# Optimization experiments

Measured on AMD Instinct MI355X. Metric: run time of the kernel, lower is better.

Reference implementation:

```python
import jax, jax.numpy as jnp
import numpy as np

N = 20000   # nodes
E = 160000  # edges
IN = 16     # in_channels
H = 32      # hidden_channels
MID = 32    # edge-MLP hidden width


def setup_inputs() -> dict:
    key = jax.random.key(0)
    ks = jax.random.split(key, 18)
    s = 0.1  # param scale
    return {
        "x": jax.random.normal(ks[0], (N, IN), jnp.float32),
        "edge_index": jax.random.randint(ks[1], (2, E), 0, N, dtype=jnp.int64),
        "edge_weight": jax.random.uniform(ks[2], (E,), jnp.float32),
        # edge_net1: Linear(1,32) -> SiLU -> Linear(32, IN*H)
        "en1_w1": jax.random.normal(ks[3], (1, MID), jnp.float32) * s,
        "en1_b1": jax.random.normal(ks[4], (MID,), jnp.float32) * s,
        "en1_w2": jax.random.normal(ks[5], (MID, IN * H), jnp.float32) * s,
        "en1_b2": jax.random.normal(ks[6], (IN * H,), jnp.float32) * s,
        "root1": jax.random.normal(ks[7], (IN, H), jnp.float32) * s,
        "bias1": jax.random.normal(ks[8], (H,), jnp.float32) * s,
        # edge_net2: Linear(1,32) -> SiLU -> Linear(32, H*H)
        "en2_w1": jax.random.normal(ks[9], (1, MID), jnp.float32) * s,
        "en2_b1": jax.random.normal(ks[10], (MID,), jnp.float32) * s,
        "en2_w2": jax.random.normal(ks[11], (MID, H * H), jnp.float32) * s,
        "en2_b2": jax.random.normal(ks[12], (H * H,), jnp.float32) * s,
        "root2": jax.random.normal(ks[13], (H, H), jnp.float32) * s,
        "bias2": jax.random.normal(ks[14], (H,), jnp.float32) * s,
        "dec_w": jax.random.normal(ks[15], (H, 1), jnp.float32) * s,
        "dec_b": jax.random.normal(ks[16], (1,), jnp.float32) * s,
    }


def _nnconv(x, src, dst, inv_cnt, e, w1, b1, w2, b2, root, bias, cin, cout):
    # edge MLP -> per-edge [cin, cout] weight matrix
    h = jax.nn.silu(e @ w1 + b1)            # [E, MID]
    w = (h @ w2 + b2).reshape(-1, cin, cout)  # [E, cin, cout]
    msg = jnp.einsum('ei,eio->eo', x[src], w)  # per-edge matmul [E, cout]
    agg = jax.ops.segment_sum(msg, dst, num_segments=N) * inv_cnt  # scatter-mean
    return agg + x @ root + bias


def reference(x, edge_index, edge_weight,
              en1_w1, en1_b1, en1_w2, en1_b2, root1, bias1,
              en2_w1, en2_b1, en2_w2, en2_b2, root2, bias2,
              dec_w, dec_b):
    src, dst = edge_index[0], edge_index[1]
    e = edge_weight[:, None]  # [E, 1]
    cnt = jax.ops.segment_sum(jnp.ones((E,), x.dtype), dst, num_segments=N)
    inv_cnt = (1.0 / jnp.maximum(cnt, 1.0))[:, None]  # [N, 1]
    h = _nnconv(x, src, dst, inv_cnt, e, en1_w1, en1_b1, en1_w2, en1_b2, root1, bias1, IN, H)
    h = jax.nn.silu(h)
    h = _nnconv(h, src, dst, inv_cnt, e, en2_w1, en2_b1, en2_w2, en2_b2, root2, bias2, H, H)
    h = jax.nn.silu(h)
    out = h @ dec_w + dec_b  # [N, 1]
    return out[:, 0]
```

## Files before the change

### kernel.cpp

```cpp
#include <hip/hip_runtime.h>
#include <hip/hip_bf16.h>

#define NN 20000
#define EE 160000
#define HH 32
#define MIDD 32

typedef _Float16 f16x4 __attribute__((ext_vector_type(4)));
typedef _Float16 f16x8 __attribute__((ext_vector_type(8)));
typedef float f32x4 __attribute__((ext_vector_type(4)));

__device__ __forceinline__ float silu_f(float v) {
    return __fdividef(v, 1.0f + __expf(-v));
}

__device__ __forceinline__ void gload_lds_b32(const void* gsrc, void* ldst) {
    __builtin_amdgcn_global_load_lds(
        (const __attribute__((address_space(1))) void*)gsrc,
        (__attribute__((address_space(3))) void*)ldst, 4, 0, 0);
}


__global__ void count_kernel(const int* __restrict__ ei, int* __restrict__ cnt) {
    int e = blockIdx.x * 256 + threadIdx.x;
    if (e < EE) atomicAdd(&cnt[ei[EE + e]], 1);
}

__global__ __launch_bounds__(1024) void scan_kernel(
    const int* __restrict__ cnt, int* __restrict__ off,
    int* __restrict__ cur, float* __restrict__ invc) {
    const int t = threadIdx.x;
    const int base = t * 20;
    __shared__ int wtot[16];

    int c[20];
    if (base + 20 <= NN) {
        const int4* p = (const int4*)(cnt + base);
        #pragma unroll
        for (int q = 0; q < 5; ++q) *(int4*)&c[4 * q] = p[q];
    } else {
        #pragma unroll
        for (int r = 0; r < 20; ++r) {
            int idx = base + r;
            c[r] = (idx < NN) ? cnt[idx] : 0;
        }
    }

    int loc[20];
    int s = 0;
    #pragma unroll
    for (int r = 0; r < 20; ++r) { loc[r] = s; s += c[r]; }

    const int lane = t & 63, wv = t >> 6;
    int incl = s;
    #pragma unroll
    for (int d2 = 1; d2 < 64; d2 <<= 1) {
        int u = __shfl_up(incl, d2);
        if (lane >= d2) incl += u;
    }
    if (lane == 63) wtot[wv] = incl;
    __syncthreads();
    int wbase = 0;
    for (int p2 = 0; p2 < wv; ++p2) wbase += wtot[p2];

    const int excl = wbase + incl - s;

    int o[20];
    #pragma unroll
    for (int r = 0; r < 20; ++r) o[r] = excl + loc[r];
    float iv[20];
    #pragma unroll
    for (int r = 0; r < 20; ++r) iv[r] = 1.0f / fmaxf((float)c[r], 1.0f);

    if (base + 20 <= NN) {
        #pragma unroll
        for (int q = 0; q < 5; ++q) {
            ((int4*)(off + base))[q]    = *(const int4*)&o[4 * q];
            ((int4*)(cur + base))[q]    = *(const int4*)&o[4 * q];
            ((float4*)(invc + base))[q] = *(const float4*)&iv[4 * q];
        }
    } else {
        #pragma unroll
        for (int r = 0; r < 20; ++r) {
            int idx = base + r;
            if (idx < NN) { off[idx] = o[r]; cur[idx] = o[r]; invc[idx] = iv[r]; }
        }
    }
    if (t == 0) off[NN] = EE;
}

__global__ void scatter_kernel(const int* __restrict__ ei, const float* __restrict__ ewt,
                               int* __restrict__ cur,
                               int* __restrict__ ssrc, float* __restrict__ sew) {
    int e = blockIdx.x * 256 + threadIdx.x;
    if (e < EE) {
        int d = ei[EE + e];
        int pos = atomicAdd(&cur[d], 1);
        ssrc[pos] = ei[e];
        sew[pos] = ewt[e];
    }
}

__global__ void build_wt(const float* __restrict__ w2a, const float* __restrict__ b2a,
                         const float* __restrict__ ra,
                         const float* __restrict__ w2b, const float* __restrict__ b2b,
                         const float* __restrict__ rb,
                         const float* __restrict__ x,
                         _Float16* __restrict__ Wt1, _Float16* __restrict__ Wt2,
                         _Float16* __restrict__ x16) {
    int idx = blockIdx.x * 256 + threadIdx.x;
    if (idx < 17408) {
        int o = idx / 544, k = idx % 544;
        float v;
        if (k < 512) {
            int m = k & 31, i = k >> 5;
            v = w2a[m * 512 + i * 32 + o];
        } else if (k < 528) {
            v = b2a[(k - 512) * 32 + o];
        } else {
            v = ra[(k - 528) * 32 + o];
        }
        Wt1[o * 544 + k] = (_Float16)v;
    } else if (idx < 52224) {
        int j = idx - 17408;
        int o = j / 1088, k = j % 1088;
        float v;
        if (k < 1024) {
            int m = k & 31, i = k >> 5;
            v = w2b[m * 1024 + i * 32 + o];
        } else if (k < 1056) {
            v = b2b[(k - 1024) * 32 + o];
        } else {
            v = rb[(k - 1056) * 32 + o];
        }
        Wt2[o * 1088 + k] = (_Float16)v;
    } else if (idx < 52224 + NN * 16) {
        int j = idx - 52224;
        x16[j] = (_Float16)x[j];
    }
}


template <int CIN, bool DECODE>
__global__ __launch_bounds__(512, 6) void fused_layer(
    const _Float16* __restrict__ xin16, const int* __restrict__ ssrc,
    const float* __restrict__ sew, const int* __restrict__ off,
    const float* __restrict__ invc, const float* __restrict__ w1,
    const float* __restrict__ b1, const _Float16* __restrict__ Wt,
    const float* __restrict__ bias, void* __restrict__ outp,
    const float* __restrict__ dw, const float* __restrict__ db) {
    constexpr int K = 34 * CIN;
    constexpr int LDK = K + 4;
    constexpr int JS = (32 * CIN) / 64;
    constexpr int NH = JS / 8;
    constexpr int steps = K / 32;
    constexpr int CAP = 192;
    constexpr int RPG = 128 / CIN;
    constexpr int LPR = CIN / 2;

    extern __shared__ char smem[];
    _Float16* Fl = (_Float16*)smem;
    float* pool = (float*)(smem + (size_t)16 * LDK * 2);
    int*   Is = (int*)pool;
    float* Es = pool + CAP;
    _Float16* Xs = (_Float16*)(pool + 2 * CAP);
    float* red = pool;

    const int t = threadIdx.x;
    const int n0 = blockIdx.x * 16;
    const int lane = t & 63, w = t >> 6;

    const int E0 = off[n0];
    const int E1 = off[n0 + 16];
    const int L = E1 - E0;
    const int Lc = (L < CAP) ? L : CAP;

    if (w == 0) {
        for (int c = 0; c < Lc; c += 64) {
            int idx = c + lane; idx = (idx < L - 1) ? idx : (L - 1);
            gload_lds_b32(ssrc + E0 + idx, Is + c);
        }
    } else if (w == 1) {
        for (int c = 0; c < Lc; c += 64) {
            int idx = c + lane; idx = (idx < L - 1) ? idx : (L - 1);
            gload_lds_b32(sew + E0 + idx, Es + c);
        }
    }
    __syncthreads();

    {
        const int G = (Lc + RPG - 1) / RPG;
        const int er = lane / LPR;
        const int ecp = lane % LPR;
        for (int p = w; p < G; p += 8) {
            int el = p * RPG + er; el = (el < Lc - 1) ? el : (Lc - 1);
            int sn = Is[el];
            gload_lds_b32(xin16 + (size_t)sn * CIN + 2 * ecp,
                          Xs + (size_t)p * RPG * CIN);
        }
    }
    __syncthreads();

    {
        const int m = lane & 31;
        const int ihalf = (lane >> 5) * JS;
        const int i0 = lane & (CIN - 1);
        const float w1v = w1[m];
        const float b1v = b1[m];

        for (int c = 0; c < 2; ++c) {
            const int nsub = w * 2 + c;
            const int d = n0 + nsub;
            float Sacc[JS];
            #pragma unroll
            for (int j = 0; j < JS; ++j) Sacc[j] = 0.f;
            float S0 = 0.f;

            const int e0l = off[d] - E0, e1l = off[d + 1] - E0;
            const int eL = (e1l < Lc) ? e1l : Lc;
            const float iv = invc[d];

            #pragma unroll 2
            for (int el = e0l; el < eL; ++el) {
                const float ew = Es[el];
                const float hv = silu_f(fmaf(ew, w1v, b1v));
                const int rb = el * CIN;
                f16x8 xh[NH];
                #pragma unroll
                for (int q = 0; q < NH; ++q)
                    xh[q] = *(const f16x8*)&Xs[rb + ihalf + 8 * q];
                #pragma unroll
                for (int q = 0; q < NH; ++q)
                    #pragma unroll
                    for (int j = 0; j < 8; ++j)
                        Sacc[8 * q + j] = fmaf((float)xh[q][j], hv, Sacc[8 * q + j]);
                S0 += (float)Xs[rb + i0];
            }
            for (int el = eL; el < e1l; ++el) {
                const int sn2 = ssrc[E0 + el];
                const float ew2 = sew[E0 + el];
                const float hv2 = silu_f(fmaf(ew2, w1v, b1v));
                const _Float16* xrow = xin16 + (size_t)sn2 * CIN;
                #pragma unroll
                for (int q = 0; q < NH; ++q) {
                    f16x8 xq = *(const f16x8*)(xrow + ihalf + 8 * q);
                    #pragma unroll
                    for (int j = 0; j < 8; ++j)
                        Sacc[8 * q + j] = fmaf((float)xq[j], hv2, Sacc[8 * q + j]);
                }
                S0 += (float)xrow[i0];
            }

            _Float16* Fr = Fl + (size_t)nsub * LDK;
            #pragma unroll
            for (int j = 0; j < JS; ++j)
                Fr[(ihalf + j) * 32 + m] = (_Float16)(Sacc[j] * iv);
            if (lane < CIN)
                Fr[32 * CIN + lane] = (_Float16)(S0 * iv);
            else if (lane < 2 * CIN)
                Fr[32 * CIN + lane] = xin16[(size_t)d * CIN + (lane - CIN)];
        }
    }
    __syncthreads();

    const int o16 = lane & 15, g = lane >> 4;

    const _Float16* Arow = Fl + (size_t)o16 * LDK + g * 4;
    const _Float16* B0 = Wt + (size_t)o16 * K + g * 4;
    const _Float16* B1 = Wt + (size_t)(o16 + 16) * K + g * 4;

    f32x4 acc0 = {0.f, 0.f, 0.f, 0.f};
    f32x4 acc1 = {0.f, 0.f, 0.f, 0.f};

    const int sb = (steps * w) >> 3;
    const int se = (steps * (w + 1)) >> 3;
    #pragma unroll 2
    for (int s = sb; s < se; ++s) {
        const int k0 = s * 32;
        f16x4 alo = *(const f16x4*)(Arow + k0);
        f16x4 ahi = *(const f16x4*)(Arow + k0 + 16);
        f16x4 b0l = *(const f16x4*)(B0 + k0);
        f16x4 b0h = *(const f16x4*)(B0 + k0 + 16);
        f16x4 b1l = *(const f16x4*)(B1 + k0);
        f16x4 b1h = *(const f16x4*)(B1 + k0 + 16);
        f16x8 a, bb0, bb1;
        #pragma unroll
        for (int j = 0; j < 4; ++j) {
            a[j] = alo[j];  a[j + 4] = ahi[j];
            bb0[j] = b0l[j]; bb0[j + 4] = b0h[j];
            bb1[j] = b1l[j]; bb1[j + 4] = b1h[j];
        }
        acc0 = __builtin_amdgcn_mfma_f32_16x16x32_f16(a, bb0, acc0, 0, 0, 0);
        acc1 = __builtin_amdgcn_mfma_f32_16x16x32_f16(a, bb1, acc1, 0, 0, 0);
    }

    if (w > 0) {
        float* rw = red + (w - 1) * 512;
        #pragma unroll
        for (int r = 0; r < 4; ++r) {
            rw[(g * 4 + r) * 32 + o16]      = acc0[r];
            rw[(g * 4 + r) * 32 + 16 + o16] = acc1[r];
        }
    }
    __syncthreads();
    if (w == 0) {
        #pragma unroll
        for (int r = 0; r < 4; ++r) {
            const int ro = (g * 4 + r) * 32 + o16;
            #pragma unroll
            for (int p = 0; p < 7; ++p) {
                acc0[r] += red[p * 512 + ro];
                acc1[r] += red[p * 512 + ro + 16];
            }
        }
        const float bb0 = bias[o16], bb1 = bias[o16 + 16];
        const int nrow = n0 + g * 4;
        if (!DECODE) {
            _Float16* op = (_Float16*)outp;
            #pragma unroll
            for (int r = 0; r < 4; ++r) {
                op[(size_t)(nrow + r) * 32 + o16]      = (_Float16)silu_f(acc0[r] + bb0);
                op[(size_t)(nrow + r) * 32 + 16 + o16] = (_Float16)silu_f(acc1[r] + bb1);
            }
        } else {
            float* op = (float*)outp;
            const float w0 = dw[o16], w1v = dw[o16 + 16];
            const float dbv = db[0];
            #pragma unroll
            for (int r = 0; r < 4; ++r) {
                float p = silu_f(acc0[r] + bb0) * w0 + silu_f(acc1[r] + bb1) * w1v;
                p += __shfl_xor(p, 1);
                p += __shfl_xor(p, 2);
                p += __shfl_xor(p, 4);
                p += __shfl_xor(p, 8);
                if (o16 == 0) op[nrow + r] = p + dbv;
            }
        }
    }
}


extern "C" void kernel_launch(void* const* d_in, const int* in_sizes, int n_in,
                              void* d_out, int out_size, void* d_ws, size_t ws_size,
                              hipStream_t stream) {
    const float* x      = (const float*)d_in[0];
    const int*   ei     = (const int*)d_in[1];
    const float* ew     = (const float*)d_in[2];
    const float* en1_w1 = (const float*)d_in[3];
    const float* en1_b1 = (const float*)d_in[4];
    const float* en1_w2 = (const float*)d_in[5];
    const float* en1_b2 = (const float*)d_in[6];
    const float* root1  = (const float*)d_in[7];
    const float* bias1  = (const float*)d_in[8];
    const float* en2_w1 = (const float*)d_in[9];
    const float* en2_b1 = (const float*)d_in[10];
    const float* en2_w2 = (const float*)d_in[11];
    const float* en2_b2 = (const float*)d_in[12];
    const float* root2  = (const float*)d_in[13];
    const float* bias2  = (const float*)d_in[14];
    const float* dec_w  = (const float*)d_in[15];
    const float* dec_b  = (const float*)d_in[16];
    float* out = (float*)d_out;
    (void)in_sizes; (void)n_in; (void)out_size; (void)ws_size;

    char* wp = (char*)d_ws;
    auto alloc = [&](size_t bytes) {
        char* p = wp;
        wp += (bytes + 255) & ~(size_t)255;
        return p;
    };
    int*      cnt  = (int*)alloc((size_t)NN * 4);
    int*      off  = (int*)alloc((size_t)(NN + 1) * 4);
    int*      cur  = (int*)alloc((size_t)NN * 4);
    float*    invc = (float*)alloc((size_t)NN * 4);
    int*      ssrc = (int*)alloc((size_t)EE * 4);
    float*    sew  = (float*)alloc((size_t)EE * 4);
    _Float16* h1h  = (_Float16*)alloc((size_t)NN * 32 * 2);
    _Float16* x16  = (_Float16*)alloc((size_t)NN * 16 * 2);
    _Float16* Wt1  = (_Float16*)alloc((size_t)17408 * 2);
    _Float16* Wt2  = (_Float16*)alloc((size_t)34816 * 2);

    hipMemsetAsync(cnt, 0, (size_t)NN * 4, stream);

    count_kernel<<<(EE + 255) / 256, 256, 0, stream>>>(ei, cnt);
    scan_kernel<<<1, 1024, 0, stream>>>(cnt, off, cur, invc);
    scatter_kernel<<<(EE + 255) / 256, 256, 0, stream>>>(ei, ew, cur, ssrc, sew);
    build_wt<<<(52224 + NN * 16 + 255) / 256, 256, 0, stream>>>(
        en1_w2, en1_b2, root1, en2_w2, en2_b2, root2, x, Wt1, Wt2, x16);

    auto f1 = fused_layer<16, false>;
    auto f2 = fused_layer<32, true>;
    (void)hipFuncSetAttribute((const void*)f1,
                              hipFuncAttributeMaxDynamicSharedMemorySize, 163840);
    (void)hipFuncSetAttribute((const void*)f2,
                              hipFuncAttributeMaxDynamicSharedMemorySize, 163840);

    const size_t lds1 = (size_t)16 * (34 * 16 + 4) * 2 + 14336;
    const size_t lds2 = (size_t)16 * (34 * 32 + 4) * 2 + 14336;

    fused_layer<16, false><<<NN / 16, 512, lds1, stream>>>(
        x16, ssrc, sew, off, invc, en1_w1, en1_b1, Wt1, bias1, h1h, nullptr, nullptr);
    fused_layer<32, true><<<NN / 16, 512, lds2, stream>>>(
        h1h, ssrc, sew, off, invc, en2_w1, en2_b1, Wt2, bias2, out, dec_w, dec_b);
}
```

Baseline: 103.3 us.

## Compute per-node edge aggregation with MFMA and interleave src/weight pairs

The per-edge outer-product accumulation (silu hidden times gathered source features) moves from scalar FMAs to 16x16x32 f16 MFMA, with edges as the reduction dimension. Source index and edge weight are packed into one int2 array so a single LDS load brings both, and the silu hidden values are precomputed into LDS. The old scalar overflow path becomes a chunked loop over edges in CAP-sized pieces. The cost is extra LDS, per-element gather and masking in the MFMA operand build, and a lower occupancy hint.

```diff
diff --git a/kernel.cpp b/kernel.cpp
--- a/kernel.cpp
+++ b/kernel.cpp
@@ -90,14 +90,12 @@
 }
 
 __global__ void scatter_kernel(const int* __restrict__ ei, const float* __restrict__ ewt,
-                               int* __restrict__ cur,
-                               int* __restrict__ ssrc, float* __restrict__ sew) {
+                               int* __restrict__ cur, int2* __restrict__ spair) {
     int e = blockIdx.x * 256 + threadIdx.x;
     if (e < EE) {
         int d = ei[EE + e];
         int pos = atomicAdd(&cur[d], 1);
-        ssrc[pos] = ei[e];
-        sew[pos] = ewt[e];
+        spair[pos] = make_int2(ei[e], __float_as_int(ewt[e]));
     }
 }
 
@@ -142,128 +140,156 @@
 
 
 template <int CIN, bool DECODE>
-__global__ __launch_bounds__(512, 6) void fused_layer(
-    const _Float16* __restrict__ xin16, const int* __restrict__ ssrc,
-    const float* __restrict__ sew, const int* __restrict__ off,
-    const float* __restrict__ invc, const float* __restrict__ w1,
-    const float* __restrict__ b1, const _Float16* __restrict__ Wt,
-    const float* __restrict__ bias, void* __restrict__ outp,
-    const float* __restrict__ dw, const float* __restrict__ db) {
+__global__ __launch_bounds__(512, 4) void fused_layer(
+    const _Float16* __restrict__ xin16, const int* __restrict__ spair,
+    const int* __restrict__ off, const float* __restrict__ invc,
+    const float* __restrict__ w1, const float* __restrict__ b1,
+    const _Float16* __restrict__ Wt, const float* __restrict__ bias,
+    void* __restrict__ outp, const float* __restrict__ dw,
+    const float* __restrict__ db) {
     constexpr int K = 34 * CIN;
     constexpr int LDK = K + 4;
-    constexpr int JS = (32 * CIN) / 64;
-    constexpr int NH = JS / 8;
     constexpr int steps = K / 32;
     constexpr int CAP = 192;
     constexpr int RPG = 128 / CIN;
     constexpr int LPR = CIN / 2;
+    constexpr int NIH = CIN / 16;
 
     extern __shared__ char smem[];
     _Float16* Fl = (_Float16*)smem;
-    float* pool = (float*)(smem + (size_t)16 * LDK * 2);
-    int*   Is = (int*)pool;
-    float* Es = pool + CAP;
-    _Float16* Xs = (_Float16*)(pool + 2 * CAP);
-    float* red = pool;
+    char* poolb = smem + (size_t)16 * LDK * 2;
+    int* Ps = (int*)poolb;
+    _Float16* Xs = (_Float16*)(poolb + (2 * CAP + 64) * 4);
+    _Float16* Hs = Xs + CAP * CIN;
+    float* red = (float*)poolb;
 
     const int t = threadIdx.x;
     const int n0 = blockIdx.x * 16;
     const int lane = t & 63, w = t >> 6;
-
-    const int E0 = off[n0];
-    const int E1 = off[n0 + 16];
+    const int col = lane & 15, g4 = (lane >> 4) * 4;
+
+    const int E0 = off[n0], E1 = off[n0 + 16];
     const int L = E1 - E0;
-    const int Lc = (L < CAP) ? L : CAP;
-
-    if (w == 0) {
-        for (int c = 0; c < Lc; c += 64) {
-            int idx = c + lane; idx = (idx < L - 1) ? idx : (L - 1);
-            gload_lds_b32(ssrc + E0 + idx, Is + c);
-        }
-    } else if (w == 1) {
-        for (int c = 0; c < Lc; c += 64) {
-            int idx = c + lane; idx = (idx < L - 1) ? idx : (L - 1);
-            gload_lds_b32(sew + E0 + idx, Es + c);
-        }
+
+    const int d0 = n0 + w * 2;
+    const int e0l0 = off[d0] - E0;
+    const int e1l0 = off[d0 + 1] - E0;
+    const int e1l1 = off[d0 + 2] - E0;
+
+    f32x4 aS[2][2][NIH];
+    f32x4 a0[2][NIH];
+    #pragma unroll
+    for (int c = 0; c < 2; ++c) {
+        #pragma unroll
+        for (int mh = 0; mh < 2; ++mh)
+            #pragma unroll
+            for (int ih = 0; ih < NIH; ++ih) aS[c][mh][ih] = (f32x4){0.f, 0.f, 0.f, 0.f};
+        #pragma unroll
+        for (int ih = 0; ih < NIH; ++ih) a0[c][ih] = (f32x4){0.f, 0.f, 0.f, 0.f};
+    }
+
+    for (int base = 0; base < L; base += CAP) {
+        const int Lc = (L - base < CAP) ? (L - base) : CAP;
+
+        for (int c = w * 64; c < 2 * Lc; c += 512) {
+            int gidx = 2 * (E0 + base) + c + lane;
+            gidx = (gidx < 2 * EE) ? gidx : (2 * EE - 1);
+            gload_lds_b32(spair + gidx, Ps + c);
+        }
+        __syncthreads();
+
+        {
+            const int G = (Lc + RPG - 1) / RPG;
+            const int er = lane / LPR, ecp = lane % LPR;
+            for (int p = w; p < G; p += 8) {
+                int el = p * RPG + er; el = (el < Lc - 1) ? el : (Lc - 1);
+                int sn = Ps[2 * el];
+                gload_lds_b32(xin16 + (size_t)sn * CIN + 2 * ecp,
+                              Xs + (size_t)p * RPG * CIN);
+            }
+        }
+        for (int idx = t; idx < Lc * 32; idx += 512) {
+            int e = idx >> 5, m = idx & 31;
+            float ew = __int_as_float(Ps[2 * e + 1]);
+            Hs[idx] = (_Float16)silu_f(fmaf(ew, w1[m], b1[m]));
+        }
+        __syncthreads();
+
+        #pragma unroll
+        for (int c = 0; c < 2; ++c) {
+            int lo = ((c == 0) ? e0l0 : e1l0) - base;
+            int hi = ((c == 0) ? e1l0 : e1l1) - base;
+            lo = (lo < 0) ? 0 : lo;
+            hi = (hi > Lc) ? Lc : hi;
+            for (int ks = lo; ks < hi; ks += 32) {
+                f16x8 bf[NIH];
+                #pragma unroll
+                for (int ih = 0; ih < NIH; ++ih)
+                    #pragma unroll
+                    for (int j = 0; j < 4; ++j) {
+                        int k1 = ks + g4 + j, k2 = k1 + 16;
+                        int c1 = (k1 < hi) ? k1 : (Lc - 1);
+                        int c2 = (k2 < hi) ? k2 : (Lc - 1);
+                        bf[ih][j]     = Xs[c1 * CIN + ih * 16 + col];
+                        bf[ih][j + 4] = Xs[c2 * CIN + ih * 16 + col];
+                    }
+                f16x8 af[2];
+                #pragma unroll
+                for (int mh = 0; mh < 2; ++mh)
+                    #pragma unroll
+                    for (int j = 0; j < 4; ++j) {
+                        int k1 = ks + g4 + j, k2 = k1 + 16;
+                        _Float16 v1 = Hs[((k1 < hi) ? k1 : (Lc - 1)) * 32 + mh * 16 + col];
+                        _Float16 v2 = Hs[((k2 < hi) ? k2 : (Lc - 1)) * 32 + mh * 16 + col];
+                        af[mh][j]     = (k1 < hi) ? v1 : (_Float16)0;
+                        af[mh][j + 4] = (k2 < hi) ? v2 : (_Float16)0;
+                    }
+                f16x8 ao;
+                #pragma unroll
+                for (int j = 0; j < 4; ++j) {
+                    int k1 = ks + g4 + j, k2 = k1 + 16;
+                    ao[j]     = (col == 0 && k1 < hi) ? (_Float16)1 : (_Float16)0;
+                    ao[j + 4] = (col == 0 && k2 < hi) ? (_Float16)1 : (_Float16)0;
+                }
+                #pragma unroll
+                for (int mh = 0; mh < 2; ++mh)
+                    #pragma unroll
+                    for (int ih = 0; ih < NIH; ++ih)
+                        aS[c][mh][ih] = __builtin_amdgcn_mfma_f32_16x16x32_f16(
+                            af[mh], bf[ih], aS[c][mh][ih], 0, 0, 0);
+                #pragma unroll
+                for (int ih = 0; ih < NIH; ++ih)
+                    a0[c][ih] = __builtin_amdgcn_mfma_f32_16x16x32_f16(
+                        ao, bf[ih], a0[c][ih], 0, 0, 0);
+            }
+        }
+        if (base + CAP < L) __syncthreads();
+    }
+
+    #pragma unroll
+    for (int c = 0; c < 2; ++c) {
+        const int d = n0 + w * 2 + c;
+        const float iv = invc[d];
+        _Float16* Fr = Fl + (size_t)(w * 2 + c) * LDK;
+        #pragma unroll
+        for (int mh = 0; mh < 2; ++mh)
+            #pragma unroll
+            for (int ih = 0; ih < NIH; ++ih)
+                #pragma unroll
+                for (int r = 0; r < 4; ++r)
+                    Fr[32 * (ih * 16 + col) + mh * 16 + g4 + r] =
+                        (_Float16)(aS[c][mh][ih][r] * iv);
+        if (g4 == 0) {
+            #pragma unroll
+            for (int ih = 0; ih < NIH; ++ih)
+                Fr[32 * CIN + ih * 16 + col] = (_Float16)(a0[c][ih][0] * iv);
+        }
+        if (lane >= CIN && lane < 2 * CIN)
+            Fr[32 * CIN + lane] = xin16[(size_t)d * CIN + (lane - CIN)];
     }
     __syncthreads();
 
-    {
-        const int G = (Lc + RPG - 1) / RPG;
-        const int er = lane / LPR;
-        const int ecp = lane % LPR;
-        for (int p = w; p < G; p += 8) {
-            int el = p * RPG + er; el = (el < Lc - 1) ? el : (Lc - 1);
-            int sn = Is[el];
-            gload_lds_b32(xin16 + (size_t)sn * CIN + 2 * ecp,
-                          Xs + (size_t)p * RPG * CIN);
-        }
-    }
-    __syncthreads();
-
-    {
-        const int m = lane & 31;
-        const int ihalf = (lane >> 5) * JS;
-        const int i0 = lane & (CIN - 1);
-        const float w1v = w1[m];
-        const float b1v = b1[m];
-
-        for (int c = 0; c < 2; ++c) {
-            const int nsub = w * 2 + c;
-            const int d = n0 + nsub;
-            float Sacc[JS];
-            #pragma unroll
-            for (int j = 0; j < JS; ++j) Sacc[j] = 0.f;
-            float S0 = 0.f;
-
-            const int e0l = off[d] - E0, e1l = off[d + 1] - E0;
-            const int eL = (e1l < Lc) ? e1l : Lc;
-            const float iv = invc[d];
-
-            #pragma unroll 2
-            for (int el = e0l; el < eL; ++el) {
-                const float ew = Es[el];
-                const float hv = silu_f(fmaf(ew, w1v, b1v));
-                const int rb = el * CIN;
-                f16x8 xh[NH];
-                #pragma unroll
-                for (int q = 0; q < NH; ++q)
-                    xh[q] = *(const f16x8*)&Xs[rb + ihalf + 8 * q];
-                #pragma unroll
-                for (int q = 0; q < NH; ++q)
-                    #pragma unroll
-                    for (int j = 0; j < 8; ++j)
-                        Sacc[8 * q + j] = fmaf((float)xh[q][j], hv, Sacc[8 * q + j]);
-                S0 += (float)Xs[rb + i0];
-            }
-            for (int el = eL; el < e1l; ++el) {
-                const int sn2 = ssrc[E0 + el];
-                const float ew2 = sew[E0 + el];
-                const float hv2 = silu_f(fmaf(ew2, w1v, b1v));
-                const _Float16* xrow = xin16 + (size_t)sn2 * CIN;
-                #pragma unroll
-                for (int q = 0; q < NH; ++q) {
-                    f16x8 xq = *(const f16x8*)(xrow + ihalf + 8 * q);
-                    #pragma unroll
-                    for (int j = 0; j < 8; ++j)
-                        Sacc[8 * q + j] = fmaf((float)xq[j], hv2, Sacc[8 * q + j]);
-                }
-                S0 += (float)xrow[i0];
-            }
-
-            _Float16* Fr = Fl + (size_t)nsub * LDK;
-            #pragma unroll
-            for (int j = 0; j < JS; ++j)
-                Fr[(ihalf + j) * 32 + m] = (_Float16)(Sacc[j] * iv);
-            if (lane < CIN)
-                Fr[32 * CIN + lane] = (_Float16)(S0 * iv);
-            else if (lane < 2 * CIN)
-                Fr[32 * CIN + lane] = xin16[(size_t)d * CIN + (lane - CIN)];
-        }
-    }
-    __syncthreads();
-
-    const int o16 = lane & 15, g = lane >> 4;
+    const int o16 = col, g = lane >> 4;
 
     const _Float16* Arow = Fl + (size_t)o16 * LDK + g * 4;
     const _Float16* B0 = Wt + (size_t)o16 * K + g * 4;
@@ -369,22 +395,21 @@
         wp += (bytes + 255) & ~(size_t)255;
         return p;
     };
-    int*      cnt  = (int*)alloc((size_t)NN * 4);
-    int*      off  = (int*)alloc((size_t)(NN + 1) * 4);
-    int*      cur  = (int*)alloc((size_t)NN * 4);
-    float*    invc = (float*)alloc((size_t)NN * 4);
-    int*      ssrc = (int*)alloc((size_t)EE * 4);
-    float*    sew  = (float*)alloc((size_t)EE * 4);
-    _Float16* h1h  = (_Float16*)alloc((size_t)NN * 32 * 2);
-    _Float16* x16  = (_Float16*)alloc((size_t)NN * 16 * 2);
-    _Float16* Wt1  = (_Float16*)alloc((size_t)17408 * 2);
-    _Float16* Wt2  = (_Float16*)alloc((size_t)34816 * 2);
+    int*      cnt   = (int*)alloc((size_t)NN * 4);
+    int*      off   = (int*)alloc((size_t)(NN + 1) * 4);
+    int*      cur   = (int*)alloc((size_t)NN * 4);
+    float*    invc  = (float*)alloc((size_t)NN * 4);
+    int2*     spair = (int2*)alloc((size_t)EE * 8);
+    _Float16* h1h   = (_Float16*)alloc((size_t)NN * 32 * 2);
+    _Float16* x16   = (_Float16*)alloc((size_t)NN * 16 * 2);
+    _Float16* Wt1   = (_Float16*)alloc((size_t)17408 * 2);
+    _Float16* Wt2   = (_Float16*)alloc((size_t)34816 * 2);
 
     hipMemsetAsync(cnt, 0, (size_t)NN * 4, stream);
 
     count_kernel<<<(EE + 255) / 256, 256, 0, stream>>>(ei, cnt);
     scan_kernel<<<1, 1024, 0, stream>>>(cnt, off, cur, invc);
-    scatter_kernel<<<(EE + 255) / 256, 256, 0, stream>>>(ei, ew, cur, ssrc, sew);
+    scatter_kernel<<<(EE + 255) / 256, 256, 0, stream>>>(ei, ew, cur, spair);
     build_wt<<<(52224 + NN * 16 + 255) / 256, 256, 0, stream>>>(
         en1_w2, en1_b2, root1, en2_w2, en2_b2, root2, x, Wt1, Wt2, x16);
 
@@ -395,11 +420,13 @@
     (void)hipFuncSetAttribute((const void*)f2,
                               hipFuncAttributeMaxDynamicSharedMemorySize, 163840);
 
-    const size_t lds1 = (size_t)16 * (34 * 16 + 4) * 2 + 14336;
-    const size_t lds2 = (size_t)16 * (34 * 32 + 4) * 2 + 14336;
+    const size_t lds1 = (size_t)16 * (34 * 16 + 4) * 2 + (448 * 4 + 192 * 16 * 2 + 192 * 64);
+    const size_t lds2 = (size_t)16 * (34 * 32 + 4) * 2 + (448 * 4 + 192 * 32 * 2 + 192 * 64);
 
     fused_layer<16, false><<<NN / 16, 512, lds1, stream>>>(
-        x16, ssrc, sew, off, invc, en1_w1, en1_b1, Wt1, bias1, h1h, nullptr, nullptr);
+        x16, (const int*)spair, off, invc, en1_w1, en1_b1, Wt1, bias1, h1h,
+        nullptr, nullptr);
     fused_layer<32, true><<<NN / 16, 512, lds2, stream>>>(
-        h1h, ssrc, sew, off, invc, en2_w1, en2_b1, Wt2, bias2, out, dec_w, dec_b);
-}
+        h1h, (const int*)spair, off, invc, en2_w1, en2_b1, Wt2, bias2, out,
+        dec_w, dec_b);
+}
```

New measurement: 99.57 us. -3.6%, faster.
